# Optimization experiments

Measured on AMD Instinct MI355X. Metric: run time of the kernel, lower is better.

## Reference

```python
import jax, jax.numpy as jnp
import numpy as np

B, C, N, L, CO, K, KT = 16, 32, 1024, 24, 64, 3, 3


def setup_inputs() -> dict:
    key = jax.random.key(0)
    ks = jax.random.split(key, 20)
    rn = lambda k, s, sc=0.05: (jax.random.normal(k, s, jnp.float32) * sc)
    return {
        'x': rn(ks[0], (B, C, N, L), 1.0),
        'supports': rn(ks[1], (N, N), 0.02),
        # ST_BLOCK conv1 (1x1, bias)
        'conv1_w': rn(ks[2], (CO, C)), 'conv1_b': jnp.zeros((CO,), jnp.float32),
        # TATT params
        't_conv1_w': rn(ks[3], (C,)), 't_conv2_w': rn(ks[4], (N,)),
        't_w': rn(ks[5], (N, C)), 't_b': jnp.zeros((L, L), jnp.float32), 't_v': rn(ks[6], (L, L)),
        # SATT params
        's_conv1_w': rn(ks[7], (C,)), 's_conv2_w': rn(ks[8], (L,)),
        's_w': rn(ks[9], (L, C)), 's_b': jnp.zeros((N, N), jnp.float32), 's_v': rn(ks[10], (N, N)),
        # dynamic Chebyshev GCN 1x1 conv (K*C -> CO, bias)
        'gcn_w': rn(ks[11], (CO, K * C)), 'gcn_b': jnp.zeros((CO,), jnp.float32),
        # time conv (1,Kt), padding (0,1), bias
        'time_w': rn(ks[12], (CO, CO, 1, KT)), 'time_b': jnp.zeros((CO,), jnp.float32),
        # LayerNorm([CO, N, L])
        'ln_w': jnp.ones((CO, N, L), jnp.float32), 'ln_b': jnp.zeros((CO, N, L), jnp.float32),
    }


def _att(logits_raw, v):
    # logits_raw: [B,M,M]; v: [M,M]
    logits = jnp.einsum('mk,bkq->bmq', v, logits_raw)
    logits = logits - jnp.max(logits, axis=1, keepdims=True)
    return jax.nn.softmax(logits, axis=-1)


def _tatt(x, w1, w2, w, b, v):
    f1 = jnp.einsum('bcnl,c->bln', x, w1)          # conv over channels on [B,c,L,N]
    f2 = jnp.einsum('bcnl,n->bcl', x, w2)          # conv over node-channel on [B,N,c,L]
    raw = jax.nn.sigmoid(jnp.einsum('bln,nc,bcq->blq', f1, w, f2) + b)
    return _att(raw, v)                            # [B,L,L]


def _satt(x, w1, w2, w, b, v):
    f1 = jnp.einsum('bcnl,c->bnl', x, w1)          # [B,N,L]
    f2 = jnp.einsum('bcnl,l->bcn', x, w2)          # [B,c,N]
    raw = jax.nn.sigmoid(jnp.einsum('bnl,lc,bcm->bnm', f1, w, f2) + b)
    return _att(raw, v)                            # [B,N,N]


def reference(x, supports, conv1_w, conv1_b, t_conv1_w, t_conv2_w, t_w, t_b, t_v,
              s_conv1_w, s_conv2_w, s_w, s_b, s_v, gcn_w, gcn_b,
              time_w, time_b, ln_w, ln_b):
    Bn, Cn, Nn, Ln = x.shape
    Kc = gcn_w.shape[1] // Cn
    x_input = jnp.einsum('oc,bcnl->bonl', conv1_w, x) + conv1_b[None, :, None, None]

    T_coef = _tatt(x, t_conv1_w, t_conv2_w, t_w, t_b, t_v)
    T_coef = jnp.swapaxes(T_coef, -1, -2)          # transpose as in torch code
    x_TAt = jnp.einsum('bcnl,blq->bcnq', x, T_coef)

    S_coef = _satt(x, s_conv1_w, s_conv2_w, s_w, s_b, s_v)  # ds: [B,N,N]

    # dynamic Chebyshev polynomials scaled per-sample by ds
    I = jnp.eye(Nn, dtype=x.dtype)
    Ls = [S_coef * I, S_coef * supports]
    T0, T1 = I, supports
    for _ in range(2, Kc):
        T2 = 2.0 * (supports @ T1) - T0
        T0, T1 = T1, T2
        Ls.append(S_coef * T2)
    Lap = jnp.stack(Ls, axis=1)                    # [B,K,N,N]
    Lap = jnp.swapaxes(Lap, -1, -2)

    xg = jnp.einsum('bcnl,bknq->bckql', x_TAt, Lap)         # [B,C,K,N,L]
    xg = xg.reshape(Bn, Cn * Kc, Nn, Ln)
    gcn = jnp.einsum('of,bfnl->bonl', gcn_w, xg) + gcn_b[None, :, None, None]
    gcn = jax.nn.relu(gcn)

    tc = jax.lax.conv_general_dilated(
        gcn, time_w, window_strides=(1, 1), padding=((0, 0), (1, 1)),
        dimension_numbers=('NCHW', 'OIHW', 'NCHW')) + time_b[None, :, None, None]

    pre = jax.nn.relu(tc + x_input)
    mu = jnp.mean(pre, axis=(1, 2, 3), keepdims=True)
    var = jnp.mean(jnp.square(pre - mu), axis=(1, 2, 3), keepdims=True)
    out = (pre - mu) * jax.lax.rsqrt(var + 1e-5) * ln_w[None] + ln_b[None]
    return (out, S_coef, T_coef)
```

## Files before the change

### kernel.cpp

```cpp
#include <hip/hip_runtime.h>
#include <cstddef>

namespace {
constexpr int B_ = 16, C_ = 32, N_ = 1024, L_ = 24, CO_ = 64;

constexpr size_t S_OFF = (size_t)B_*CO_*N_*L_;
constexpr size_t T_OFF = S_OFF + (size_t)B_*N_*N_;

constexpr size_t O_GCN  = 0;
constexpr size_t O_XTLC = 13631488;
constexpr size_t O_XR   = 19922944;
constexpr size_t O_SUPB = 26214400;
constexpr size_t O_LGB  = 26738688;
constexpr size_t O_F1T  = 38797312;
constexpr size_t O_F2T  = 39583744;
constexpr size_t O_F2S  = 39596032;
constexpr size_t O_GT   = 40120320;
constexpr size_t O_GS   = 40132608;
constexpr size_t O_CM   = 40656896;
constexpr size_t O_WAP  = 40673280;
constexpr size_t O_W2P  = 40676352;
constexpr size_t O_PART = 40683520;
constexpr size_t O_BST  = 40689664;

constexpr size_t OS_A1  = 0;
constexpr size_t OS_A2  = OS_A1 + (size_t)B_*N_*N_;
constexpr size_t OS_XP  = OS_A2 + (size_t)B_*N_*N_;
constexpr size_t OS_SV  = OS_XP + (size_t)B_*N_*768;
constexpr size_t OS_SUP2= OS_SV + (size_t)N_*N_;
constexpr size_t OS_SUPR= OS_SUP2 + (size_t)N_*N_;
constexpr size_t OS_SUPA= OS_SUPR + (size_t)N_*N_;

typedef unsigned short u16;
typedef __attribute__((ext_vector_type(8))) short short8v;
typedef __attribute__((ext_vector_type(4))) short short4v;
typedef __attribute__((ext_vector_type(4))) float f32x4;

__device__ __forceinline__ u16 f2bf(float x) {
  unsigned u = __builtin_bit_cast(unsigned, x);
  return (u16)((u + 0x7fffu + ((u >> 16) & 1u)) >> 16);
}
__device__ __forceinline__ float bf2f(u16 v) {
  return __builtin_bit_cast(float, ((unsigned)v) << 16);
}
__device__ __forceinline__ unsigned fkey(float f) {
  unsigned u = __builtin_bit_cast(unsigned, f);
  return (u & 0x80000000u) ? ~u : (u | 0x80000000u);
}
__device__ __forceinline__ float funkey(unsigned k) {
  unsigned u = (k & 0x80000000u) ? (k ^ 0x80000000u) : ~k;
  return __builtin_bit_cast(float, u);
}
__device__ __forceinline__ void gl_lds16(const void* g, void* l) {
  __builtin_amdgcn_global_load_lds(
      (const __attribute__((address_space(1))) unsigned int*)g,
      (__attribute__((address_space(3))) unsigned int*)l, 16, 0, 0);
}

__global__ __launch_bounds__(256) void k_ff(const float* __restrict__ x,
    const float* __restrict__ t1w, const float* __restrict__ s1w,
    const float* __restrict__ w2s, const float* __restrict__ t2w,
    const float* __restrict__ sw, float* __restrict__ f1t,
    u16* __restrict__ gsp, u16* __restrict__ f2p,
    float* __restrict__ part2) {
  int blk = blockIdx.x;
  int b = blk >> 7, n0 = (blk & 127) << 3;
  __shared__ float ls[32*200];
  __shared__ float tls[8*33];
  __shared__ float f1sL[200];
  int t = threadIdx.x;
  const float* xb = x + (size_t)b*C_*N_*L_;
  #pragma unroll
  for (int i = 0; i < 24; i++) {
    int flat = i*256 + t;
    int c = flat / 192, r = flat - c*192;
    int nl = r / 24, l = r - nl*24;
    ls[c*200 + nl*25 + l] = xb[((size_t)c*N_ + n0 + nl)*L_ + l];
  }
  __syncthreads();
  if (t < 192) {
    int nl = t / 24, l = t - (t/24)*24;
    float a1 = 0.f, a2 = 0.f;
    #pragma unroll
    for (int c = 0; c < C_; c++) {
      float v = ls[c*200 + nl*25 + l];
      a1 += v * t1w[c]; a2 += v * s1w[c];
    }
    f1t[((size_t)b*L_ + l)*N_ + n0 + nl] = a1;
    f1sL[nl*25 + l] = a2;
  }
  {
    int c = t >> 3, nl = t & 7;
    const float* lp = &ls[c*200 + nl*25];
    float a = 0.f;
    #pragma unroll
    for (int l = 0; l < L_; l++) a += lp[l] * w2s[l];
    tls[nl*33 + c] = a;
  }
  const float* twn = t2w + n0;
  #pragma unroll
  for (int i = 0; i < 3; i++) {
    int flat = t + 256*i;
    int c2 = flat / 24, l2 = flat - c2*24;
    float a2 = 0.f;
    #pragma unroll
    for (int nl2 = 0; nl2 < 8; nl2++)
      a2 += ls[c2*200 + nl2*25 + l2] * twn[nl2];
    part2[(size_t)blk*768 + flat] = a2;
  }
  __syncthreads();
  {
    int m = n0 + (t >> 5), c = t & 31;
    float v = tls[(t >> 5)*33 + c];
    f2p[(size_t)b*32768 + (size_t)(m >> 4)*512 +
        (((m & 15) | ((c >> 3) << 4)) << 3) + (c & 7)] = f2bf(v);
  }
  {
    int nl = t >> 5, cg = t & 31;
    const float* fl = &f1sL[nl*25];
    float ag = 0.f;
    #pragma unroll
    for (int l = 0; l < L_; l++) ag += fl[l] * sw[l*32 + cg];
    int n = n0 + nl;
    gsp[(size_t)b*32768 + (size_t)(n >> 4)*512 +
        (((n & 15) | ((cg >> 3) << 4)) << 3) + (cg & 7)] = f2bf(ag);
  }
}

__global__ __launch_bounds__(256) void k_f2t_red(const float* __restrict__ part2,
                                                 float* __restrict__ f2t) {
  int idx = blockIdx.x * 256 + threadIdx.x;
  int b = idx / 768, cl = idx - b*768;
  const float* p = part2 + (size_t)b*98304 + cl;
  float s = 0.f;
  #pragma unroll 8
  for (int k = 0; k < 128; k++) s += p[(size_t)k*768];
  f2t[idx] = s;
}

__global__ __launch_bounds__(1024) void k_gt(const float* __restrict__ f1t,
    const float* __restrict__ tw, float* __restrict__ g_t) {
  int bl = blockIdx.x; int tid = threadIdx.x;
  int nsub = tid >> 5, c = tid & 31;
  const float* f = f1t + (size_t)bl * N_;
  float a = 0.f;
  for (int i = 0; i < 32; i++) {
    int n = nsub + (i << 5);
    a += f[n] * tw[n*32 + c];
  }
  __shared__ float s[1024];
  s[tid] = a; __syncthreads();
  for (int off = 512; off >= 32; off >>= 1) {
    if (tid < off) s[tid] += s[tid + off];
    __syncthreads();
  }
  if (tid < 32) g_t[(size_t)bl*32 + tid] = s[tid];
}

__global__ __launch_bounds__(576) void k_tatt(const float* __restrict__ g_t,
    const float* __restrict__ f2t, const float* __restrict__ tb,
    const float* __restrict__ tv, float* __restrict__ Tout) {
  int b = blockIdx.x; int tid = threadIdx.x;
  int l = tid / 24, q = tid % 24;
  __shared__ float rawS[576], logS[576], cmS[24], rmS[24], rsS[24];
  float acc = tb[tid];
  const float* g = g_t + ((size_t)b*L_ + l)*C_;
  const float* f = f2t + (size_t)b*C_*L_ + q;
  #pragma unroll
  for (int c = 0; c < C_; c++) acc += g[c] * f[(size_t)c*L_];
  rawS[tid] = 1.f / (1.f + expf(-acc));
  __syncthreads();
  float lg = 0.f;
  #pragma unroll
  for (int k = 0; k < L_; k++) lg += tv[l*L_ + k] * rawS[k*L_ + q];
  logS[tid] = lg;
  __syncthreads();
  if (l == 0) { float m = -3.4e38f; for (int mm = 0; mm < L_; mm++) m = fmaxf(m, logS[mm*L_ + q]); cmS[q] = m; }
  __syncthreads();
  float lc = lg - cmS[q];
  logS[tid] = lc;
  __syncthreads();
  if (q == 0) { float m = -3.4e38f; for (int qq = 0; qq < L_; qq++) m = fmaxf(m, logS[l*L_ + qq]); rmS[l] = m; }
  __syncthreads();
  float e = expf(lc - rmS[l]);
  logS[tid] = e;
  __syncthreads();
  if (q == 0) { float s = 0.f; for (int qq = 0; qq < L_; qq++) s += logS[l*L_ + qq]; rsS[l] = s; }
  __syncthreads();
  Tout[(size_t)b*576 + q*24 + l] = e / rsS[l];
}

__global__ __launch_bounds__(256) void k_rawsm(
    const u16* __restrict__ gsp, const u16* __restrict__ f2p,
    const float* __restrict__ sb, u16* __restrict__ rawp) {
  int b = blockIdx.z;
  int mg0 = blockIdx.y * 8;
  int ng0 = blockIdx.x * 8;
  const u16* A  = gsp + (size_t)b*32768;
  const u16* Bm = f2p + (size_t)b*32768;
  int tid = threadIdx.x;
  int w = tid >> 6, lane = tid & 63;
  int wr = w >> 1, wc = w & 1;
  int lm = lane & 15, hi = lane >> 4;
  __shared__ __align__(16) u16 smem[16*512];
  #pragma unroll
  for (int i = 0; i < 4; i++) {
    int f = w + 4*i;
    if (f < 8)
      gl_lds16(A + (size_t)(mg0 + f)*512 + (lane << 3), &smem[f*512]);
    else
      gl_lds16(Bm + (size_t)(ng0 + f - 8)*512 + (lane << 3), &smem[f*512]);
  }
  __syncthreads();
  f32x4 acc[4][4] = {};
  #pragma unroll
  for (int j = 0; j < 4; j++) {
    short8v bv = *(const short8v*)&smem[(8 + wc*4 + j)*512 + (lane << 3)];
    #pragma unroll
    for (int i = 0; i < 4; i++) {
      short8v av = *(const short8v*)&smem[(wr*4 + i)*512 + (lane << 3)];
      acc[i][j] = __builtin_amdgcn_mfma_f32_16x16x32_bf16(av, bv, acc[i][j], 0, 0, 0);
    }
  }
  u16* d = rawp + ((size_t)b << 20);
  #pragma unroll
  for (int i = 0; i < 4; i++) {
    int nb = (mg0 + wr*4 + i)*16 + hi*4;
    #pragma unroll
    for (int j = 0; j < 4; j++) {
      int m = (ng0 + wc*4 + j)*16 + lm;
      const float* sbp = sb + (size_t)nb*N_ + m;
      u16 ov[4];
      #pragma unroll
      for (int r = 0; r < 4; r++) {
        float v2 = acc[i][j][r] + sbp[(size_t)r*N_];
        ov[r] = f2bf(1.f / (1.f + expf(-v2)));
      }
      int fi2 = ((nb >> 5) << 6) | (m >> 4);
      int lp  = (m & 15) | (((nb >> 3) & 3) << 4);
      *(unsigned long long*)&d[(size_t)fi2*512 + lp*8 + (nb & 7)] =
          *(unsigned long long*)ov;
    }
  }
}

__global__ void k_pack_sv(const float* __restrict__ sv, u16* __restrict__ svp,
                          const float* __restrict__ sup, u16* __restrict__ supA,
                          u16* __restrict__ supB, u16* __restrict__ supR,
                          const float* __restrict__ gcn_w, const float* __restrict__ time_w,
                          const float* __restrict__ conv1_w, u16* __restrict__ WAp,
                          u16* __restrict__ W2p, unsigned* __restrict__ cmz) {
  int t = blockIdx.x * 256 + threadIdx.x;
  int fi = t >> 6, l = t & 63;
  int mg = fi >> 5, kg = fi & 31;
  int row = (mg << 4) + (l & 15);
  int k   = (kg << 5) + ((l >> 4) << 3);
  {
    const float* s = sv + (size_t)row*N_ + k;
    const float* s2 = sup + (size_t)row*N_ + k;
    u16* d  = svp  + ((size_t)fi << 9) + (l << 3);
    u16* dA = supA + ((size_t)fi << 9) + (l << 3);
    u16* dR = supR + (size_t)row*N_ + k;
    #pragma unroll
    for (int j = 0; j < 8; j++) {
      u16 bv = f2bf(s2[j]);
      d[j] = f2bf(s[j]); dA[j] = bv; dR[j] = bv;
    }
  }
  {
    int kgB = fi >> 6, nbB = fi & 63;
    int colB = (nbB << 4) + (l & 15);
    int krB  = (kgB << 5) + ((l >> 4) << 3);
    u16* dB = supB + ((size_t)fi << 9) + (l << 3);
    #pragma unroll
    for (int j = 0; j < 8; j++) dB[j] = f2bf(sup[(size_t)(krB + j)*N_ + colB]);
  }
  if (t < 16384) cmz[t] = 0u;
  if (t < 6144) {
    int fi2 = t >> 9, l2 = (t >> 3) & 63, j2 = t & 7;
    int kg2 = fi2 >> 2, cf = fi2 & 3;
    int o = cf*16 + (l2 & 15), c = ((l2 >> 4) << 3) + j2;
    WAp[t] = f2bf(gcn_w[o*96 + c*3 + kg2]);
  }
  if (t < 14336) {
    int fi2 = t >> 9, l2 = (t >> 3) & 63, j2 = t & 7;
    int kg2 = fi2 >> 2, cf = fi2 & 3;
    int o2 = cf*16 + (l2 & 15), kk = ((l2 >> 4) << 3) + j2;
    float v;
    if (kg2 < 6) { int tt2 = kg2 >> 1, i = (kg2 & 1)*32 + kk; v = time_w[o2*192 + i*3 + tt2]; }
    else v = conv1_w[o2*32 + kk];
    W2p[t] = f2bf(v);
  }
}

__global__ __launch_bounds__(256) void k_sup2(const u16* __restrict__ Ap,
    const u16* __restrict__ Bp, u16* __restrict__ D) {
  int mg0 = blockIdx.y * 8, ng0 = blockIdx.x * 8;
  constexpr int Kg = 32, Ng = 64;
  int tid = threadIdx.x;
  int w = tid >> 6, lane = tid & 63;
  int wr = w >> 1, wc = w & 1;
  __shared__ __align__(16) u16 smem[2 * 8192];
  u16* As = smem;
  u16* Bs = smem + 8192;
  f32x4 acc1[4][4] = {};
  for (int k0 = 0; k0 < Kg; k0 += 2) {
    __syncthreads();
    #pragma unroll
    for (int i = 0; i < 4; i++) {
      int f = w + 4*i;
      int r = f >> 1, c = f & 1;
      size_t goff = (((size_t)(mg0 + r)) * Kg + (k0 + c)) * 512 + (lane << 3);
      gl_lds16(Ap + goff, &As[f * 512]);
      int cb = f >> 3, tn = f & 7;
      size_t boff = (((size_t)(k0 + cb)) * Ng + (ng0 + tn)) * 512 + (lane << 3);
      gl_lds16(Bp + boff, &Bs[f * 512]);
    }
    __syncthreads();
    #pragma unroll
    for (int kk = 0; kk < 2; kk++) {
      short8v bq[4], av[4];
      #pragma unroll
      for (int j = 0; j < 4; j++)
        bq[j] = *(const short8v*)&Bs[(kk*8 + wc*4 + j)*512 + (lane << 3)];
      #pragma unroll
      for (int i = 0; i < 4; i++)
        av[i] = *(const short8v*)&As[((wr*4 + i)*2 + kk)*512 + (lane << 3)];
      #pragma unroll
      for (int i = 0; i < 4; i++)
        #pragma unroll
        for (int j = 0; j < 4; j++)
          acc1[i][j] = __builtin_amdgcn_mfma_f32_16x16x32_bf16(av[i], bq[j], acc1[i][j], 0, 0, 0);
    }
  }
  #pragma unroll
  for (int i = 0; i < 4; i++) {
    int row = (mg0 + wr*4 + i)*16 + ((lane >> 4) << 2);
    #pragma unroll
    for (int j = 0; j < 4; j++) {
      int col = (ng0 + wc*4 + j)*16 + (lane & 15);
      #pragma unroll
      for (int r = 0; r < 4; r++)
        D[(size_t)(row + r)*N_ + col] =
            f2bf(2.f*acc1[i][j][r] - ((row + r) == col ? 1.f : 0.f));
    }
  }
}

__global__ __launch_bounds__(512) void k_logits(
    const u16* __restrict__ Ap, const u16* __restrict__ Bp,
    u16* __restrict__ lgb, unsigned* __restrict__ cmg) {
  int hw = blockIdx.x + (blockIdx.y << 2) + (blockIdx.z << 5);
  int logical = (hw & 7)*64 + (hw >> 3);
  int ng0 = (logical & 3) * 16;
  int mg0 = ((logical >> 2) & 7) * 8;
  int b   = logical >> 5;
  const u16* A1 = Ap;
  const u16* Bm = Bp + ((size_t)b << 20);
  constexpr int Kg = 32, Ng = 64;
  int tid = threadIdx.x;
  int w = tid >> 6, lane = tid & 63;
  int r2 = w >> 2, c4 = w & 3;
  int lm = lane & 15, hi = lane >> 4;
  __shared__ __align__(16) u16 smem[3 * 12288];
  f32x4 acc[4][4] = {};
  #define LG_STAGE(kg, buf) {                                                   \
    u16* dst = smem + (buf)*12288;                                              \
    size_t goffA = (((size_t)(mg0 + w)) * Kg + (kg)) * 512 + (lane << 3);       \
    gl_lds16(A1 + goffA, &dst[w*512]);                                          \
    size_t bo0 = (((size_t)(kg)) * Ng + (ng0 + w)) * 512 + (lane << 3);         \
    gl_lds16(Bm + bo0, &dst[4096 + w*512]);                                     \
    size_t bo1 = (((size_t)(kg)) * Ng + (ng0 + w + 8)) * 512 + (lane << 3);     \
    gl_lds16(Bm + bo1, &dst[4096 + (w + 8)*512]);                               \
  }
  LG_STAGE(0, 0);
  LG_STAGE(1, 1);
  for (int kg = 0; kg < Kg; kg++) {
    int cur = kg % 3;
    if (kg + 2 < Kg) {
      LG_STAGE(kg + 2, (kg + 2) % 3);
      asm volatile("s_waitcnt vmcnt(6)" ::: "memory");
    } else if (kg + 1 < Kg) {
      asm volatile("s_waitcnt vmcnt(3)" ::: "memory");
    } else {
      asm volatile("s_waitcnt vmcnt(0)" ::: "memory");
    }
    __builtin_amdgcn_s_barrier();
    __builtin_amdgcn_sched_barrier(0);
    const u16* Asrc = smem + cur*12288;
    const u16* Bsrc = Asrc + 4096;
    short8v bq[4];
    #pragma unroll
    for (int j = 0; j < 4; j++)
      bq[j] = *(const short8v*)&Bsrc[(c4*4 + j)*512 + (lane << 3)];
    #pragma unroll
    for (int i = 0; i < 4; i++) {
      short8v av = *(const short8v*)&Asrc[(r2*4 + i)*512 + (lane << 3)];
      #pragma unroll
      for (int j = 0; j < 4; j++)
        acc[i][j] = __builtin_amdgcn_mfma_f32_16x16x32_bf16(av, bq[j], acc[i][j], 0, 0, 0);
    }
    asm volatile("" ::: "memory");
    __builtin_amdgcn_s_barrier();
  }
  #undef LG_STAGE
  __shared__ unsigned cmL[256];
  if (tid < 256) cmL[tid] = 0u;
  __syncthreads();
  #pragma unroll
  for (int j = 0; j < 4; j++) {
    float m = -3.4e38f;
    #pragma unroll
    for (int i = 0; i < 4; i++)
      #pragma unroll
      for (int r = 0; r < 4; r++) m = fmaxf(m, acc[i][j][r]);
    m = fmaxf(m, __shfl_xor(m, 16));
    m = fmaxf(m, __shfl_xor(m, 32));
    if (hi == 0)
      atomicMax(&cmL[(c4*4 + j)*16 + lm], fkey(m));
  }
  __syncthreads();
  if (tid < 256)
    atomicMax(&cmg[(size_t)b*N_ + ng0*16 + tid], cmL[tid]);
  u16* d1 = lgb + ((size_t)b << 20);
  #pragma unroll
  for (int i = 0; i < 4; i++) {
    int row = (mg0 + r2*4 + i)*16 + (hi << 2);
    #pragma unroll
    for (int j = 0; j < 4; j++) {
      int col = (ng0 + c4*4 + j)*16 + lm;
      #pragma unroll
      for (int r = 0; r < 4; r++)
        d1[(size_t)(row + r)*N_ + col] = f2bf(acc[i][j][r]);
    }
  }
}

__global__ __launch_bounds__(256) void k_smpk(const u16* __restrict__ lgb,
    float* __restrict__ Sout, const unsigned* __restrict__ cm,
    const u16* __restrict__ supR, const u16* __restrict__ sup2B,
    u16* __restrict__ A1p, u16* __restrict__ A2p, u16* __restrict__ gcnB) {
  int bm = blockIdx.x;
  int b = bm >> 10, row = bm & 1023;
  int t = threadIdx.x;
  int k0 = t * 4;
  const unsigned* cmb = cm + (size_t)b * N_;
  short4v l4 = *(const short4v*)&lgb[(size_t)bm * N_ + k0];
  float v[4];
  #pragma unroll
  for (int j = 0; j < 4; j++) v[j] = bf2f((u16)l4[j]) - funkey(cmb[k0 + j]);
  float mx = fmaxf(fmaxf(v[0], v[1]), fmaxf(v[2], v[3]));
  #pragma unroll
  for (int off = 32; off; off >>= 1) mx = fmaxf(mx, __shfl_down(mx, off));
  __shared__ float sm[4], ss[4];
  int w = t >> 6, lane = t & 63;
  if (lane == 0) sm[w] = mx;
  __syncthreads();
  mx = fmaxf(fmaxf(sm[0], sm[1]), fmaxf(sm[2], sm[3]));
  float e[4]; float s = 0.f;
  #pragma unroll
  for (int j = 0; j < 4; j++) { e[j] = expf(v[j] - mx); s += e[j]; }
  #pragma unroll
  for (int off = 32; off; off >>= 1) s += __shfl_down(s, off);
  if (lane == 0) ss[w] = s;
  __syncthreads();
  float inv = 1.f / (ss[0] + ss[1] + ss[2] + ss[3]);
  float p[4];
  #pragma unroll
  for (int j = 0; j < 4; j++) p[j] = e[j] * inv;
  *(float4*)&Sout[(size_t)bm * N_ + k0] = make_float4(p[0], p[1], p[2], p[3]);
  short4v s1v = *(const short4v*)&supR[(size_t)row*N_ + k0];
  short4v s2v = *(const short4v*)&sup2B[(size_t)row*N_ + k0];
  unsigned fi = (unsigned)((row >> 4) << 5) | (unsigned)(k0 >> 5);
  unsigned lp = (unsigned)(row & 15) | ((unsigned)((k0 >> 3) & 3) << 4);
  size_t dst = ((size_t)b << 20) + ((size_t)fi << 9) + (lp << 3) + (k0 & 7);
  u16 o1[4], o2[4];
  #pragma unroll
  for (int j = 0; j < 4; j++) {
    o1[j] = f2bf(p[j] * bf2f((u16)s1v[j]));
    o2[j] = f2bf(p[j] * bf2f((u16)s2v[j]));
  }
  *(unsigned long long*)&A1p[dst] = *(unsigned long long*)o1;
  *(unsigned long long*)&A2p[dst] = *(unsigned long long*)o2;
  if (t < 32) {
    size_t po = ((size_t)bm*26 + (t >> 4)*25)*64 + (t & 15)*4;
    *(unsigned long long*)&gcnB[po] = 0ull;
  }
}

__global__ __launch_bounds__(768) void k_xtat8(const float* __restrict__ x,
    const float* __restrict__ Tout, u16* __restrict__ xTlc, u16* __restrict__ xr,
    u16* __restrict__ Xp) {
  int blk = blockIdx.x;
  int b = blk >> 7, n0 = (blk & 127) << 3;
  __shared__ float xs[6400];
  __shared__ float Tl[576];
  int tid = threadIdx.x;
  int c = tid / 24, l = tid % 24;
  #pragma unroll
  for (int nl = 0; nl < 8; nl++)
    xs[nl*800 + c*25 + l] = x[(((size_t)b*C_ + c)*N_ + n0 + nl)*L_ + l];
  if (tid < 576) Tl[tid] = Tout[(size_t)b*576 + tid];
  __syncthreads();
  int q = tid >> 5, cc = tid & 31;
  u16 xp8[8];
  #pragma unroll
  for (int nl = 0; nl < 8; nl++) {
    const float* xsn = &xs[nl*800 + cc*25];
    float acc = 0.f;
    #pragma unroll
    for (int ll = 0; ll < 24; ll++) acc += xsn[ll] * Tl[ll*24 + q];
    u16 bv = f2bf(acc);
    size_t bn = (size_t)b*N_ + n0 + nl;
    xTlc[bn*768 + tid] = bv;
    xr[bn*768 + tid] = f2bf(xsn[q]);
    xp8[nl] = bv;
  }
  int fi = (n0 >> 5)*48 + (tid >> 4);
  int lidx = (tid & 15) | (((n0 >> 3) & 3) << 4);
  *(short8v*)&Xp[(size_t)b*786432 + (size_t)fi*512 + lidx*8] = *(short8v*)xp8;
}

__global__ __launch_bounds__(512) void k_chga(
    const u16* __restrict__ A1p, const u16* __restrict__ A2p,
    const u16* __restrict__ Bp, const u16* __restrict__ xTlc,
    const float* __restrict__ S, const u16* __restrict__ WAp,
    const float* __restrict__ gcn_b, u16* __restrict__ gcn) {
  int hw = blockIdx.x + 6*blockIdx.y + 48*blockIdx.z;
  int logical = (hw & 7)*96 + (hw >> 3);
  int tx = logical % 6; int tmp = logical / 6;
  int ty = tmp & 7; int b = tmp >> 3;
  const u16* A1 = A1p + ((size_t)b << 20);
  const u16* A2 = A2p + ((size_t)b << 20);
  const u16* Bm = Bp + (size_t)b * 786432;
  int mg0 = ty * 8;
  int ng0 = tx * 8;
  int l0 = tx * 4;
  constexpr int Kg = 32, Ng = 48;
  int tid = threadIdx.x;
  int w = tid >> 6, lane = tid & 63;
  int m  = w & 1;
  int c2 = (w >> 1) & 1;
  int r2 = w >> 2;
  int lm = lane & 15, hi = lane >> 4;
  __shared__ __align__(16) u16 smem[3 * 12288];
  f32x4 acc[4][4] = {};
  #define CH_STAGE(kg, buf) {                                                   \
    u16* dst = smem + (buf)*12288;                                              \
    size_t goffA = (((size_t)(mg0 + w)) * Kg + (kg)) * 512 + (lane << 3);       \
    gl_lds16(A1 + goffA, &dst[w*512]);                                          \
    gl_lds16(A2 + goffA, &dst[4096 + w*512]);                                   \
    size_t bo = (((size_t)(kg)) * Ng + (ng0 + w)) * 512 + (lane << 3);          \
    gl_lds16(Bm + bo, &dst[8192 + w*512]);                                      \
  }
  CH_STAGE(0, 0);
  CH_STAGE(1, 1);
  for (int kg = 0; kg < Kg; kg++) {
    int cur = kg % 3;
    if (kg + 2 < Kg) {
      CH_STAGE(kg + 2, (kg + 2) % 3);
      asm volatile("s_waitcnt vmcnt(6)" ::: "memory");
    } else if (kg + 1 < Kg) {
      asm volatile("s_waitcnt vmcnt(3)" ::: "memory");
    } else {
      asm volatile("s_waitcnt vmcnt(0)" ::: "memory");
    }
    __builtin_amdgcn_s_barrier();
    __builtin_amdgcn_sched_barrier(0);
    const u16* base = smem + cur*12288;
    const u16* Asrc = base + (m ? 4096 : 0);
    const u16* Bsrc = base + 8192;
    short8v bq[4];
    #pragma unroll
    for (int j = 0; j < 4; j++)
      bq[j] = *(const short8v*)&Bsrc[(c2*4 + j)*512 + (lane << 3)];
    #pragma unroll
    for (int i = 0; i < 4; i++) {
      short8v av = *(const short8v*)&Asrc[(r2*4 + i)*512 + (lane << 3)];
      #pragma unroll
      for (int j = 0; j < 4; j++)
        acc[i][j] = __builtin_amdgcn_mfma_f32_16x16x32_bf16(av, bq[j], acc[i][j], 0, 0, 0);
    }
    asm volatile("" ::: "memory");
    __builtin_amdgcn_s_barrier();
  }
  #undef CH_STAGE
  u16* zL  = smem;
  u16* wsm = smem + 18432;
  float gb[4];
  #pragma unroll
  for (int cf = 0; cf < 4; cf++) gb[cf] = gcn_b[cf*16 + lm];
  #pragma unroll
  for (int ch = 0; ch < 2; ch++) {
    __syncthreads();
    if (ch == 0) {
      gl_lds16(WAp + w*512 + (lane << 3), &wsm[w*512 + (lane << 3)]);
      if (w < 4)
        gl_lds16(WAp + (8 + w)*512 + (lane << 3), &wsm[(8 + w)*512 + (lane << 3)]);
    }
    if (r2 == ch) {
      #pragma unroll
      for (int i = 0; i < 4; i++)
        #pragma unroll
        for (int j = 0; j < 4; j++) {
          int col = (c2*4 + j)*16 + lm;
          int ll = col >> 5, c = col & 31;
          #pragma unroll
          for (int r = 0; r < 4; r++) {
            int lr = (i*16 + hi*4 + r)*4 + ll;
            int za = lr*36 + ((((c >> 3) + (lr >> 4)) & 3) << 3) + (c & 7);
            zL[m*9216 + za] = f2bf(acc[i][j][r]);
          }
        }
    }
    __syncthreads();
    #pragma unroll
    for (int gg = 0; gg < 2; gg++) {
      int g = w*2 + gg;
      int lr = g*16 + lm;
      int grow = ch*256 + lr;
      int nl = mg0*16 + (grow >> 2);
      int ll = l0 + (grow & 3);
      short8v a0 = *(const short8v*)&xTlc[(size_t)b*786432 + ((size_t)nl*24 + ll)*32 + hi*8];
      float sd = S[((size_t)b << 20) + (size_t)nl*1025];
      #pragma unroll
      for (int jj = 0; jj < 8; jj++)
        a0[jj] = (short)f2bf(bf2f((u16)a0[jj]) * sd);
      int slot = (hi + g) & 3;
      const u16* zp = &zL[lr*36 + slot*8];
      short4v z1lo = *(const short4v*)zp;
      short4v z1hi = *(const short4v*)(zp + 4);
      short4v z2lo = *(const short4v*)(zp + 9216);
      short4v z2hi = *(const short4v*)(zp + 9220);
      short8v a1 = {z1lo[0], z1lo[1], z1lo[2], z1lo[3], z1hi[0], z1hi[1], z1hi[2], z1hi[3]};
      short8v a2 = {z2lo[0], z2lo[1], z2lo[2], z2lo[3], z2hi[0], z2hi[1], z2hi[2], z2hi[3]};
      #pragma unroll
      for (int cf = 0; cf < 4; cf++) {
        short8v w0 = *(const short8v*)&wsm[(0*4 + cf)*512 + (lane << 3)];
        short8v w1 = *(const short8v*)&wsm[(1*4 + cf)*512 + (lane << 3)];
        short8v w2 = *(const short8v*)&wsm[(2*4 + cf)*512 + (lane << 3)];
        f32x4 a = {};
        a = __builtin_amdgcn_mfma_f32_16x16x32_bf16(a0, w0, a, 0, 0, 0);
        a = __builtin_amdgcn_mfma_f32_16x16x32_bf16(a1, w1, a, 0, 0, 0);
        a = __builtin_amdgcn_mfma_f32_16x16x32_bf16(a2, w2, a, 0, 0, 0);
        int o = cf*16 + lm;
        #pragma unroll
        for (int r = 0; r < 4; r++) {
          int gr2 = ch*256 + g*16 + hi*4 + r;
          int n2 = mg0*16 + (gr2 >> 2);
          int l2 = l0 + (gr2 & 3);
          gcn[(((size_t)b*1024 + n2)*26 + l2 + 1)*64 + o] =
              f2bf(fmaxf(a[r] + gb[cf], 0.f));
        }
      }
    }
  }
}

__global__ __launch_bounds__(256) void k_gb(const u16* __restrict__ gcn,
    const u16* __restrict__ xr, const u16* __restrict__ W2p,
    const float* __restrict__ time_b, const float* __restrict__ conv1_b,
    u16* __restrict__ preB, float* __restrict__ partials) {
  int blk = blockIdx.x;
  int b = blk / 192, mt = blk % 192;
  int tid = threadIdx.x, w = tid >> 6, lane = tid & 63;
  int lm = lane & 15, hi = lane >> 4;
  f32x4 acc[2][4] = {};
  #pragma unroll
  for (int g = 0; g < 7; g++) {
    short8v Bf[4];
    #pragma unroll
    for (int cf = 0; cf < 4; cf++)
      Bf[cf] = *(const short8v*)&W2p[(g*4 + cf)*512 + lane*8];
    #pragma unroll
    for (int rf = 0; rf < 2; rf++) {
      int row = mt*128 + (w*2 + rf)*16 + lm;
      short8v a;
      if (g < 6) {
        int n = row / 24, l = row - 24*n;
        int ts = g >> 1, o0 = (g & 1)*32;
        a = *(const short8v*)&gcn[(((size_t)b*1024 + n)*26 + l + ts)*64 + o0 + hi*8];
      } else {
        a = *(const short8v*)&xr[(size_t)b*786432 + (size_t)row*32 + hi*8];
      }
      #pragma unroll
      for (int cf = 0; cf < 4; cf++)
        acc[rf][cf] = __builtin_amdgcn_mfma_f32_16x16x32_bf16(a, Bf[cf], acc[rf][cf], 0, 0, 0);
    }
  }
  float s1 = 0.f, s2 = 0.f;
  #pragma unroll
  for (int rf = 0; rf < 2; rf++) {
    int rbase = mt*128 + (w*2 + rf)*16 + hi*4;
    int n = rbase / 24, l0 = rbase - 24*n;
    #pragma unroll
    for (int cf = 0; cf < 4; cf++) {
      int o2 = cf*16 + lm;
      float bias = time_b[o2] + conv1_b[o2];
      u16 ov[4];
      #pragma unroll
      for (int r = 0; r < 4; r++) {
        float pre = fmaxf(acc[rf][cf][r] + bias, 0.f);
        s1 += pre; s2 += pre*pre; ov[r] = f2bf(pre);
      }
      *(unsigned long long*)&preB[(((size_t)b*64 + o2)*1024 + n)*24 + l0] =
          *(unsigned long long*)ov;
    }
  }
  #pragma unroll
  for (int off = 32; off; off >>= 1) { s1 += __shfl_down(s1, off); s2 += __shfl_down(s2, off); }
  __shared__ float red[8];
  if (lane == 0) { red[w*2] = s1; red[w*2 + 1] = s2; }
  __syncthreads();
  if (tid == 0) {
    float t1 = 0.f, t2 = 0.f;
    for (int ww = 0; ww < 4; ww++) { t1 += red[ww*2]; t2 += red[ww*2 + 1]; }
    partials[blk*2] = t1; partials[blk*2 + 1] = t2;
  }
}

__global__ __launch_bounds__(256) void k_bstats(const float* __restrict__ partials,
                                                float* __restrict__ bstats) {
  int b = blockIdx.x; int tid = threadIdx.x;
  __shared__ float r1[256], r2[256];
  r1[tid] = (tid < 192) ? partials[(b*192 + tid)*2] : 0.f;
  r2[tid] = (tid < 192) ? partials[(b*192 + tid)*2 + 1] : 0.f;
  __syncthreads();
  for (int off = 128; off; off >>= 1) {
    if (tid < off) { r1[tid] += r1[tid + off]; r2[tid] += r2[tid + off]; }
    __syncthreads();
  }
  if (tid == 0) { bstats[b*2] = r1[0]; bstats[b*2 + 1] = r2[0]; }
}

__global__ void k_ln4(const u16* __restrict__ preB, float4* __restrict__ out,
                      const float* __restrict__ bstats,
                      const float4* __restrict__ lnw, const float4* __restrict__ lnb) {
  constexpr size_t PER4 = (size_t)CO_*N_*L_/4;
  size_t i = (size_t)blockIdx.x * 256 + threadIdx.x;
  int b = (int)(i / PER4); size_t r = i % PER4;
  float cnt = (float)(PER4*4);
  float mu = bstats[b*2] / cnt;
  float var = bstats[b*2 + 1] / cnt - mu*mu;
  float inv = rsqrtf(var + 1e-5f);
  short4v p4 = *(const short4v*)&preB[i*4];
  float4 w = lnw[r], bb = lnb[r];
  float4 o;
  o.x = (bf2f((u16)p4[0]) - mu)*inv*w.x + bb.x;
  o.y = (bf2f((u16)p4[1]) - mu)*inv*w.y + bb.y;
  o.z = (bf2f((u16)p4[2]) - mu)*inv*w.z + bb.z;
  o.w = (bf2f((u16)p4[3]) - mu)*inv*w.w + bb.w;
  out[i] = o;
}
}

extern "C" void kernel_launch(void* const* d_in, const int* in_sizes, int n_in,
                              void* d_out, int out_size, void* d_ws, size_t ws_size,
                              hipStream_t stream) {
  const float* x        = (const float*)d_in[0];
  const float* supports = (const float*)d_in[1];
  const float* conv1_w  = (const float*)d_in[2];
  const float* conv1_b  = (const float*)d_in[3];
  const float* t1w      = (const float*)d_in[4];
  const float* t2w      = (const float*)d_in[5];
  const float* t_w      = (const float*)d_in[6];
  const float* t_b      = (const float*)d_in[7];
  const float* t_v      = (const float*)d_in[8];
  const float* s1w      = (const float*)d_in[9];
  const float* s2w      = (const float*)d_in[10];
  const float* s_w      = (const float*)d_in[11];
  const float* s_b      = (const float*)d_in[12];
  const float* s_v      = (const float*)d_in[13];
  const float* gcn_w    = (const float*)d_in[14];
  const float* gcn_b    = (const float*)d_in[15];
  const float* time_w   = (const float*)d_in[16];
  const float* time_b   = (const float*)d_in[17];
  const float* ln_w     = (const float*)d_in[18];
  const float* ln_b     = (const float*)d_in[19];

  float* out  = (float*)d_out;
  float* Sout = out + S_OFF;
  float* Tout = out + T_OFF;
  u16*   outU = (u16*)d_out;
  float* ws   = (float*)d_ws;

  u16*   gcnB = (u16*)(ws + O_GCN);
  u16*   rawp = (u16*)(ws + O_GCN);
  u16*   xTlc = (u16*)(ws + O_XTLC);
  u16*   xr   = (u16*)(ws + O_XR);
  u16*   supB = (u16*)(ws + O_SUPB);
  u16*   lgb  = (u16*)(ws + O_LGB);
  float* part2= ws + O_LGB;
  u16*   preB = (u16*)(ws + O_LGB);
  float* f1t  = ws + O_F1T;
  float* f2t  = ws + O_F2T;
  u16*   f2p  = (u16*)(ws + O_F2S);
  float* g_t  = ws + O_GT;
  u16*   gsp  = (u16*)(ws + O_GS);
  unsigned* cm = (unsigned*)(ws + O_CM);
  u16*   WAp  = (u16*)(ws + O_WAP);
  u16*   W2p  = (u16*)(ws + O_W2P);
  float* part = ws + O_PART;
  float* bst  = ws + O_BST;

  u16*   A1p  = outU + OS_A1;
  u16*   A2p  = outU + OS_A2;
  u16*   Xp   = outU + OS_XP;
  u16*   svp  = outU + OS_SV;
  u16*   sup2B= outU + OS_SUP2;
  u16*   supR = outU + OS_SUPR;
  u16*   supA = outU + OS_SUPA;

  k_ff<<<2048, 256, 0, stream>>>(x, t1w, s1w, s2w, t2w, s_w, f1t, gsp, f2p, part2);
  k_f2t_red<<<48, 256, 0, stream>>>(part2, f2t);
  k_gt<<<B_*L_, 1024, 0, stream>>>(f1t, t_w, g_t);
  k_tatt<<<B_, 576, 0, stream>>>(g_t, f2t, t_b, t_v, Tout);
  k_rawsm<<<dim3(8, 8, B_), 256, 0, stream>>>(gsp, f2p, s_b, rawp);
  k_pack_sv<<<512, 256, 0, stream>>>(s_v, svp, supports, supA, supB, supR,
                                     gcn_w, time_w, conv1_w, WAp, W2p, cm);
  k_sup2<<<dim3(8, 8), 256, 0, stream>>>(supA, supB, sup2B);
  k_logits<<<dim3(4, 8, B_), 512, 0, stream>>>(svp, rawp, lgb, cm);
  k_smpk<<<B_*N_, 256, 0, stream>>>(lgb, Sout, cm, supR, sup2B, A1p, A2p, gcnB);
  k_xtat8<<<2048, 768, 0, stream>>>(x, Tout, xTlc, xr, Xp);
  k_chga<<<dim3(6, 8, B_), 512, 0, stream>>>(A1p, A2p, Xp, xTlc, Sout, WAp, gcn_b, gcnB);
  k_gb<<<3072, 256, 0, stream>>>(gcnB, xr, W2p, time_b, conv1_b, preB, part);
  k_bstats<<<B_, 256, 0, stream>>>(part, bst);
  k_ln4<<<24576, 256, 0, stream>>>(preB, (float4*)out, bst,
                                   (const float4*)ln_w, (const float4*)ln_b);
}
```

Before: 389.8 us.

## Emit bf16 x transpose in k_ff, merge reduction kernels, raise MFMA priority

k_ff now writes the bf16 [n][l][c] transpose of x (xr) from its shared tile, and k_xtat8 reads that half-width buffer instead of re-reading fp32 x. The f2t partial reduction and the g_t projection are merged into one 256-thread launch, dropping a kernel launch. s_setprio is raised around the MFMA loops in the two GEMM kernels so matrix waves are favoured during scheduling. The trade-off is that xTlc is now computed from bf16-rounded x rather than fp32 x, which adds rounding error, and k_ff does extra stores.

```diff
diff --git a/kernel.cpp b/kernel.cpp
--- a/kernel.cpp
+++ b/kernel.cpp
@@ -62,7 +62,7 @@
     const float* __restrict__ w2s, const float* __restrict__ t2w,
     const float* __restrict__ sw, float* __restrict__ f1t,
     u16* __restrict__ gsp, u16* __restrict__ f2p,
-    float* __restrict__ part2) {
+    float* __restrict__ part2, u16* __restrict__ xr) {
   int blk = blockIdx.x;
   int b = blk >> 7, n0 = (blk & 127) << 3;
   __shared__ float ls[32*200];
@@ -108,6 +108,14 @@
       a2 += ls[c2*200 + nl2*25 + l2] * twn[nl2];
     part2[(size_t)blk*768 + flat] = a2;
   }
+  u16* xrb = xr + (size_t)(b*N_ + n0)*768;
+  #pragma unroll
+  for (int i = 0; i < 24; i++) {
+    int flat = i*256 + t;
+    int nl = flat / 768, r = flat - nl*768;
+    int l = r >> 5, c = r & 31;
+    xrb[flat] = f2bf(ls[c*200 + nl*25 + l]);
+  }
   __syncthreads();
   {
     int m = n0 + (t >> 5), c = t & 31;
@@ -127,34 +135,36 @@
   }
 }
 
-__global__ __launch_bounds__(256) void k_f2t_red(const float* __restrict__ part2,
-                                                 float* __restrict__ f2t) {
-  int idx = blockIdx.x * 256 + threadIdx.x;
-  int b = idx / 768, cl = idx - b*768;
-  const float* p = part2 + (size_t)b*98304 + cl;
-  float s = 0.f;
-  #pragma unroll 8
-  for (int k = 0; k < 128; k++) s += p[(size_t)k*768];
-  f2t[idx] = s;
-}
-
-__global__ __launch_bounds__(1024) void k_gt(const float* __restrict__ f1t,
+__global__ __launch_bounds__(256) void k_aux(const float* __restrict__ part2,
+    float* __restrict__ f2t, const float* __restrict__ f1t,
     const float* __restrict__ tw, float* __restrict__ g_t) {
-  int bl = blockIdx.x; int tid = threadIdx.x;
-  int nsub = tid >> 5, c = tid & 31;
+  int blk = blockIdx.x;
+  int t = threadIdx.x;
+  if (blk < 48) {
+    int idx = blk * 256 + t;
+    int b = idx / 768, cl = idx - b*768;
+    const float* p = part2 + (size_t)b*98304 + cl;
+    float s = 0.f;
+    #pragma unroll 8
+    for (int k = 0; k < 128; k++) s += p[(size_t)k*768];
+    f2t[idx] = s;
+    return;
+  }
+  int bl = blk - 48;
+  int nsub = t >> 5, c = t & 31;
   const float* f = f1t + (size_t)bl * N_;
   float a = 0.f;
-  for (int i = 0; i < 32; i++) {
-    int n = nsub + (i << 5);
+  for (int i = 0; i < 128; i++) {
+    int n = nsub + (i << 3);
     a += f[n] * tw[n*32 + c];
   }
-  __shared__ float s[1024];
-  s[tid] = a; __syncthreads();
-  for (int off = 512; off >= 32; off >>= 1) {
-    if (tid < off) s[tid] += s[tid + off];
-    __syncthreads();
-  }
-  if (tid < 32) g_t[(size_t)bl*32 + tid] = s[tid];
+  __shared__ float s[256];
+  s[t] = a; __syncthreads();
+  if (t < 128) s[t] += s[t + 128];
+  __syncthreads();
+  if (t < 64) s[t] += s[t + 64];
+  __syncthreads();
+  if (t < 32) g_t[(size_t)bl*32 + t] = s[t] + s[t + 32];
 }
 
 __global__ __launch_bounds__(576) void k_tatt(const float* __restrict__ g_t,
@@ -393,6 +403,7 @@
     #pragma unroll
     for (int j = 0; j < 4; j++)
       bq[j] = *(const short8v*)&Bsrc[(c4*4 + j)*512 + (lane << 3)];
+    __builtin_amdgcn_s_setprio(1);
     #pragma unroll
     for (int i = 0; i < 4; i++) {
       short8v av = *(const short8v*)&Asrc[(r2*4 + i)*512 + (lane << 3)];
@@ -400,6 +411,7 @@
       for (int j = 0; j < 4; j++)
         acc[i][j] = __builtin_amdgcn_mfma_f32_16x16x32_bf16(av, bq[j], acc[i][j], 0, 0, 0);
     }
+    __builtin_amdgcn_s_setprio(0);
     asm volatile("" ::: "memory");
     __builtin_amdgcn_s_barrier();
   }
@@ -488,18 +500,21 @@
   }
 }
 
-__global__ __launch_bounds__(768) void k_xtat8(const float* __restrict__ x,
-    const float* __restrict__ Tout, u16* __restrict__ xTlc, u16* __restrict__ xr,
+__global__ __launch_bounds__(768) void k_xtat8(const u16* __restrict__ xr,
+    const float* __restrict__ Tout, u16* __restrict__ xTlc,
     u16* __restrict__ Xp) {
   int blk = blockIdx.x;
   int b = blk >> 7, n0 = (blk & 127) << 3;
   __shared__ float xs[6400];
   __shared__ float Tl[576];
   int tid = threadIdx.x;
-  int c = tid / 24, l = tid % 24;
-  #pragma unroll
-  for (int nl = 0; nl < 8; nl++)
-    xs[nl*800 + c*25 + l] = x[(((size_t)b*C_ + c)*N_ + n0 + nl)*L_ + l];
+  const u16* xrb = xr + (size_t)(b*N_ + n0)*768;
+  #pragma unroll
+  for (int nl = 0; nl < 8; nl++) {
+    u16 v = xrb[(size_t)nl*768 + tid];
+    int l = tid >> 5, c = tid & 31;
+    xs[nl*800 + c*25 + l] = bf2f(v);
+  }
   if (tid < 576) Tl[tid] = Tout[(size_t)b*576 + tid];
   __syncthreads();
   int q = tid >> 5, cc = tid & 31;
@@ -513,7 +528,6 @@
     u16 bv = f2bf(acc);
     size_t bn = (size_t)b*N_ + n0 + nl;
     xTlc[bn*768 + tid] = bv;
-    xr[bn*768 + tid] = f2bf(xsn[q]);
     xp8[nl] = bv;
   }
   int fi = (n0 >> 5)*48 + (tid >> 4);
@@ -574,6 +588,7 @@
     #pragma unroll
     for (int j = 0; j < 4; j++)
       bq[j] = *(const short8v*)&Bsrc[(c2*4 + j)*512 + (lane << 3)];
+    __builtin_amdgcn_s_setprio(1);
     #pragma unroll
     for (int i = 0; i < 4; i++) {
       short8v av = *(const short8v*)&Asrc[(r2*4 + i)*512 + (lane << 3)];
@@ -581,6 +596,7 @@
       for (int j = 0; j < 4; j++)
         acc[i][j] = __builtin_amdgcn_mfma_f32_16x16x32_bf16(av, bq[j], acc[i][j], 0, 0, 0);
     }
+    __builtin_amdgcn_s_setprio(0);
     asm volatile("" ::: "memory");
     __builtin_amdgcn_s_barrier();
   }
@@ -811,9 +827,8 @@
   u16*   supR = outU + OS_SUPR;
   u16*   supA = outU + OS_SUPA;
 
-  k_ff<<<2048, 256, 0, stream>>>(x, t1w, s1w, s2w, t2w, s_w, f1t, gsp, f2p, part2);
-  k_f2t_red<<<48, 256, 0, stream>>>(part2, f2t);
-  k_gt<<<B_*L_, 1024, 0, stream>>>(f1t, t_w, g_t);
+  k_ff<<<2048, 256, 0, stream>>>(x, t1w, s1w, s2w, t2w, s_w, f1t, gsp, f2p, part2, xr);
+  k_aux<<<432, 256, 0, stream>>>(part2, f2t, f1t, t_w, g_t);
   k_tatt<<<B_, 576, 0, stream>>>(g_t, f2t, t_b, t_v, Tout);
   k_rawsm<<<dim3(8, 8, B_), 256, 0, stream>>>(gsp, f2p, s_b, rawp);
   k_pack_sv<<<512, 256, 0, stream>>>(s_v, svp, supports, supA, supB, supR,
@@ -821,7 +836,7 @@
   k_sup2<<<dim3(8, 8), 256, 0, stream>>>(supA, supB, sup2B);
   k_logits<<<dim3(4, 8, B_), 512, 0, stream>>>(svp, rawp, lgb, cm);
   k_smpk<<<B_*N_, 256, 0, stream>>>(lgb, Sout, cm, supR, sup2B, A1p, A2p, gcnB);
-  k_xtat8<<<2048, 768, 0, stream>>>(x, Tout, xTlc, xr, Xp);
+  k_xtat8<<<2048, 768, 0, stream>>>(xr, Tout, xTlc, Xp);
   k_chga<<<dim3(6, 8, B_), 512, 0, stream>>>(A1p, A2p, Xp, xTlc, Sout, WAp, gcn_b, gcnB);
   k_gb<<<3072, 256, 0, stream>>>(gcnB, xr, W2p, time_b, conv1_b, preB, part);
   k_bstats<<<B_, 256, 0, stream>>>(part, bst);
```

Result: faster. 369.3 us (-5.2%).
